# Optimization experiments

Hardware: AMD Instinct MI355X
Metric: run time of the kernel (lower is better)

Reference implementation:

```python
import jax, jax.numpy as jnp
import numpy as np

WINDOW_SIZES = (4, 16, 64)
MEMORY_DIM = 256


def setup_inputs() -> dict:
    key = jax.random.key(0)
    ks = jax.random.split(key, 9)
    d_model, mem = 256, MEMORY_DIM
    s_in = 1.0 / np.sqrt(d_model)
    s_mem = 1.0 / np.sqrt(mem)
    return {
        "hidden_states": jax.random.normal(ks[0], (2, 4096, d_model), dtype=jnp.float32),
        # weights stored as (in, out) so projection is x @ W + b
        "Wq": jax.random.normal(ks[1], (d_model, mem), dtype=jnp.float32) * s_in,
        "bq": jax.random.normal(ks[2], (mem,), dtype=jnp.float32) * 0.02,
        "Wk": jax.random.normal(ks[3], (d_model, mem), dtype=jnp.float32) * s_in,
        "bk": jax.random.normal(ks[4], (mem,), dtype=jnp.float32) * 0.02,
        "Wv": jax.random.normal(ks[5], (d_model, mem), dtype=jnp.float32) * s_in,
        "bv": jax.random.normal(ks[6], (mem,), dtype=jnp.float32) * 0.02,
        "Wo": jax.random.normal(ks[7], (mem, d_model), dtype=jnp.float32) * s_mem,
        "bo": jax.random.normal(ks[8], (d_model,), dtype=jnp.float32) * 0.02,
    }


def _gather_patches(h, window):
    # h: (B, L, D). Causal window of `window` positions ending at each l,
    # zero-padded on the left (matches F.pad + unfold in the torch module).
    B, L, D = h.shape
    w = min(window, L)
    padded = jnp.pad(h, ((0, 0), (w - 1, 0), (0, 0)))  # (B, L+w-1, D)
    idx = jnp.arange(L)[:, None] + jnp.arange(w)[None, :]  # (L, w)
    return padded[:, idx]  # (B, L, w, D)


def reference(hidden_states, Wq, bq, Wk, bk, Wv, bv, Wo, bo):
    scale = 1.0 / np.sqrt(MEMORY_DIM)
    q = hidden_states @ Wq + bq  # (B, L, M)
    contexts = []
    for window in WINDOW_SIZES:
        patches = _gather_patches(hidden_states, window)  # (B, L, w, D)
        keys = patches @ Wk + bk      # (B, L, w, M)
        values = patches @ Wv + bv    # (B, L, w, M)
        scores = jnp.einsum('bld,blwd->blw', q, keys) * scale
        attn = jax.nn.softmax(scores, axis=-1)
        contexts.append(jnp.einsum('blw,blwd->bld', attn, values))
    merged = contexts[0]
    for c in contexts[1:]:
        merged = merged + c
    merged = merged / len(contexts)
    return hidden_states + merged @ Wo + bo
```

## Files before the change

### kernel.cpp

```cpp
#include <hip/hip_runtime.h>
#include <hip/hip_bf16.h>

#define D 256
#define NROWS 8192
#define LXV 4176
#define VPAD 64
#define KXFB 1064960

#define QBLK 16
#define SSTR 84
#define PSTR 104
#define MSTR 264
#define BSTR 264

typedef unsigned int u32;
typedef unsigned short u16;

typedef short bf16x8 __attribute__((ext_vector_type(8)));
typedef float f32x4 __attribute__((ext_vector_type(4)));

__device__ __forceinline__ u16 f2bf(float f) {
    u32 x = __float_as_uint(f);
    x += 0x7fffu + ((x >> 16) & 1u);
    return (u16)(x >> 16);
}
__device__ __forceinline__ u32 pk2(float a, float b) {
    return (u32)f2bf(a) | ((u32)f2bf(b) << 16);
}

__global__ __launch_bounds__(256) void qkv_mfma(
    const float* __restrict__ H,
    const float* __restrict__ Wq, const float* __restrict__ Wk,
    const float* __restrict__ Wv, const float* __restrict__ Wo,
    const float* __restrict__ bq, const float* __restrict__ bkb,
    const float* __restrict__ bvb,
    u16* __restrict__ Qf, u16* __restrict__ Kxf, u16* __restrict__ Vt,
    u16* __restrict__ WoTf)
{
    __shared__ u16 As[64 * 256];
    __shared__ u16 Bs[64 * BSTR];
    __shared__ u16 Eb[64 * 72];

    const int tid = threadIdx.x;
    const int by = blockIdx.x;
    const int bx = blockIdx.y;
    const int mat = bx >> 2;
    const int n0 = (bx & 3) * 64;
    const int row0 = by * 256;
    const int batch = by >> 4;
    const int lrow0 = row0 & 4095;
    const float* __restrict__ W = (mat == 0) ? Wq : (mat == 1) ? Wk : Wv;
    const float* __restrict__ bias = (mat == 0) ? bq : (mat == 1) ? bkb : bvb;

    const int lane = tid & 63, w = tid >> 6;
    const int l15 = lane & 15, lhi = lane >> 4;
    const int rt2 = (w & 1) * 2, ct2 = (w >> 1) * 2;

    {
        const int kp = tid & 31, ng = tid >> 5;
        u32* bd = (u32*)Bs;
        #pragma unroll
        for (int s = 0; s < 4; ++s) {
            const float* wr = W + (size_t)(s * 64 + 2 * kp) * 256 + n0 + ng * 8;
            float4 a0 = *(const float4*)(wr);
            float4 a1 = *(const float4*)(wr + 4);
            float4 b0 = *(const float4*)(wr + 256);
            float4 b1 = *(const float4*)(wr + 260);
            bd[(ng * 8 + 0) * 132 + s * 32 + kp] = pk2(a0.x, b0.x);
            bd[(ng * 8 + 1) * 132 + s * 32 + kp] = pk2(a0.y, b0.y);
            bd[(ng * 8 + 2) * 132 + s * 32 + kp] = pk2(a0.z, b0.z);
            bd[(ng * 8 + 3) * 132 + s * 32 + kp] = pk2(a0.w, b0.w);
            bd[(ng * 8 + 4) * 132 + s * 32 + kp] = pk2(a1.x, b1.x);
            bd[(ng * 8 + 5) * 132 + s * 32 + kp] = pk2(a1.y, b1.y);
            bd[(ng * 8 + 6) * 132 + s * 32 + kp] = pk2(a1.z, b1.z);
            bd[(ng * 8 + 7) * 132 + s * 32 + kp] = pk2(a1.w, b1.w);
        }
    }
    {
        const int r = tid >> 2, cb = (tid & 3) * 64;
        const float* hp = H + (size_t)(row0 + r) * 256 + cb;
        const int swz = (r & 7) << 3;
        #pragma unroll
        for (int i = 0; i < 16; ++i) {
            float4 h4 = *(const float4*)(hp + i * 4);
            uint2 pv; pv.x = pk2(h4.x, h4.y); pv.y = pk2(h4.z, h4.w);
            *(uint2*)(As + ((r * 256 + cb + i * 4) ^ swz)) = pv;
        }
    }
    __syncthreads();

    for (int t = 0; t < 4; ++t) {
        f32x4 acc[2][2];
        #pragma unroll
        for (int rr = 0; rr < 2; ++rr)
            #pragma unroll
            for (int cc = 0; cc < 2; ++cc)
                acc[rr][cc] = (f32x4){0.f, 0.f, 0.f, 0.f};
        #pragma unroll
        for (int rr = 0; rr < 2; ++rr) {
            const int rowa = (rt2 + rr) * 16 + l15;
            const int swa = (rowa & 7) << 3;
            bf16x8 af[8];
            #pragma unroll
            for (int ks = 0; ks < 8; ++ks)
                af[ks] = *(const bf16x8*)(As + ((rowa * 256 + ks * 32 + lhi * 8) ^ swa));
            #pragma unroll
            for (int ks = 0; ks < 8; ++ks)
                #pragma unroll
                for (int cc = 0; cc < 2; ++cc) {
                    bf16x8 bf = *(const bf16x8*)&Bs[((ct2 + cc) * 16 + l15) * BSTR + ks * 32 + lhi * 8];
                    acc[rr][cc] = __builtin_amdgcn_mfma_f32_16x16x32_bf16(af[ks], bf, acc[rr][cc], 0, 0, 0);
                }
        }
        __syncthreads();

        if (mat == 2) {
            #pragma unroll
            for (int cc = 0; cc < 2; ++cc) {
                const int dl = (ct2 + cc) * 16 + l15;
                const float bi = bvb[n0 + dl];
                #pragma unroll
                for (int rr = 0; rr < 2; ++rr)
                    #pragma unroll
                    for (int reg = 0; reg < 4; ++reg)
                        Eb[dl * 72 + (rt2 + rr) * 16 + lhi * 4 + reg] = f2bf(acc[rr][cc][reg] + bi);
            }
        } else {
            #pragma unroll
            for (int cc = 0; cc < 2; ++cc) {
                const int cl = (ct2 + cc) * 16 + l15;
                const float bi = bias[n0 + cl];
                #pragma unroll
                for (int rr = 0; rr < 2; ++rr)
                    #pragma unroll
                    for (int reg = 0; reg < 4; ++reg)
                        Eb[((rt2 + rr) * 16 + lhi * 4 + reg) * 72 + cl] = f2bf(acc[rr][cc][reg] + bi);
            }
        }
        if (t < 3) {
            const int r = tid >> 2, cb = (tid & 3) * 64;
            const float* hp = H + (size_t)(row0 + (t + 1) * 64 + r) * 256 + cb;
            const int swz = (r & 7) << 3;
            #pragma unroll
            for (int i = 0; i < 16; ++i) {
                float4 h4 = *(const float4*)(hp + i * 4);
                uint2 pv; pv.x = pk2(h4.x, h4.y); pv.y = pk2(h4.z, h4.w);
                *(uint2*)(As + ((r * 256 + cb + i * 4) ^ swz)) = pv;
            }
        }
        __syncthreads();

        if (mat == 2) {
            const int d2 = tid >> 2, q = tid & 3;
            uint4 v0 = *(const uint4*)&Eb[d2 * 72 + q * 16];
            uint4 v1 = *(const uint4*)&Eb[d2 * 72 + q * 16 + 8];
            u16* dst = Vt + ((size_t)batch * 256 + n0 + d2) * LXV + VPAD + lrow0 + t * 64 + q * 16;
            *(uint4*)dst = v0;
            *(uint4*)(dst + 8) = v1;
        } else {
            const int r2 = tid >> 2, c16 = (tid & 3) * 16;
            int rtile, rl;
            u16* base;
            if (mat == 0) {
                const int grow = row0 + t * 64 + r2;
                rtile = grow >> 4; rl = grow & 15;
                base = Qf;
            } else {
                const int prow = VPAD + lrow0 + t * 64 + r2;
                rtile = prow >> 4; rl = prow & 15;
                base = Kxf + (size_t)batch * KXFB;
            }
            #pragma unroll
            for (int h = 0; h < 2; ++h) {
                const int gcol = n0 + c16 + h * 8;
                const int ksq = gcol >> 5;
                const int lhq = (gcol >> 3) & 3;
                uint4 v = *(const uint4*)&Eb[r2 * 72 + c16 + h * 8];
                *(uint4*)&base[((size_t)rtile * 8 + ksq) * 512 + (rl * 4 + lhq) * 8] = v;
            }
        }
    }

    if (bx == 0 && by < 16) {
        float* Tf = (float*)As;
        const int tr = by >> 2, tc = by & 3;
        __syncthreads();
        {
            const int r = tid >> 2, c0 = (tid & 3) * 16;
            const float* src = Wo + (size_t)(tr * 64 + r) * 256 + tc * 64 + c0;
            #pragma unroll
            for (int i = 0; i < 4; ++i) {
                float4 v = *(const float4*)(src + i * 4);
                Tf[r * 68 + c0 + i * 4 + 0] = v.x;
                Tf[r * 68 + c0 + i * 4 + 1] = v.y;
                Tf[r * 68 + c0 + i * 4 + 2] = v.z;
                Tf[r * 68 + c0 + i * 4 + 3] = v.w;
            }
        }
        __syncthreads();
        {
            const int n = tid >> 2, k0 = (tid & 3) * 16;
            const int gcol = tc * 64 + n;
            const int colt = gcol >> 4, cl = gcol & 15;
            const int gk = tr * 64 + k0;
            const int ksw = gk >> 5;
            const int lhw = (gk >> 3) & 3;
            u32 pw[8];
            #pragma unroll
            for (int i = 0; i < 8; ++i)
                pw[i] = pk2(Tf[(k0 + 2 * i) * 68 + n], Tf[(k0 + 2 * i + 1) * 68 + n]);
            u16* base = WoTf + ((size_t)colt * 8 + ksw) * 512 + (cl * 4 + lhw) * 8;
            *(uint4*)base = *(uint4*)&pw[0];
            *(uint4*)(base + 8) = *(uint4*)&pw[4];
        }
    }
    if (bx == 4 && (by & 15) == 0) {
        const int batch2 = by >> 4;
        const int ks = tid >> 5, u = tid & 31;
        const u16 val = f2bf(bkb[ks * 32 + u]);
        u16* base = Kxf + (size_t)batch2 * KXFB;
        #pragma unroll
        for (int pt = 0; pt < 4; ++pt)
            #pragma unroll
            for (int rl = 0; rl < 16; ++rl)
                base[((size_t)pt * 8 + ks) * 512 + rl * 32 + u] = val;
    }
    if (bx == 8 && (by & 15) == 0) {
        const int batch2 = by >> 4;
        const u16 val = f2bf(bvb[tid]);
        const u32 vv = (u32)val | ((u32)val << 16);
        uint4 o; o.x = vv; o.y = vv; o.z = vv; o.w = vv;
        u16* dst = Vt + ((size_t)batch2 * 256 + tid) * LXV;
        #pragma unroll
        for (int j = 0; j < 8; ++j) *(uint4*)(dst + j * 8) = o;
    }
}

__global__ __launch_bounds__(256) void attn_out(
    const u16* __restrict__ Qf, const u16* __restrict__ Kxf,
    const u16* __restrict__ Vt, const u16* __restrict__ WoTf,
    const float* __restrict__ bo, const float* __restrict__ H,
    float* __restrict__ out)
{
    __shared__ float Sb[QBLK * SSTR];
    __shared__ u16 Pb[QBLK * PSTR];
    __shared__ u16 Ml[QBLK * MSTR];

    const int tid = threadIdx.x;
    const int lane = tid & 63, w = tid >> 6;
    const int l15 = lane & 15, lhi = lane >> 4;
    const int bid = blockIdx.x;
    const int r0 = (((bid & 7) << 6) + (bid >> 3)) * QBLK;
    const int batch = r0 >> 12;
    const int lb0 = r0 & 4095;

    const float scale = 0.0625f;
    const int fidx = (l15 * 4 + lhi) * 8;
    const u16* qp = Qf + (size_t)(r0 >> 4) * 4096 + fidx;
    bf16x8 qf[8];
    #pragma unroll
    for (int ks = 0; ks < 8; ++ks) qf[ks] = *(const bf16x8*)(qp + ks * 512);

    const u16* kfb = Kxf + (size_t)batch * KXFB + (size_t)(lb0 >> 4) * 4096 + fidx;
    for (int T = w; T < 5; T += 4) {
        const u16* kp = kfb + (size_t)T * 4096;
        f32x4 acc = (f32x4){0.f, 0.f, 0.f, 0.f};
        #pragma unroll
        for (int ks = 0; ks < 8; ++ks) {
            bf16x8 kf = *(const bf16x8*)(kp + ks * 512);
            acc = __builtin_amdgcn_mfma_f32_16x16x32_bf16(qf[ks], kf, acc, 0, 0, 0);
        }
        #pragma unroll
        for (int reg = 0; reg < 4; ++reg)
            Sb[(lhi * 4 + reg) * SSTR + T * 16 + l15] = acc[reg] * scale;
    }
    __syncthreads();

    {
        const int ri = w * 4 + lhi;
        const int jb = l15;
        float s5[5];
        float m = -1e30f;
        #pragma unroll
        for (int c = 0; c < 5; ++c) {
            const int j = jb + 16 * c;
            const float x = Sb[ri * SSTR + j];
            const bool v = (j >= ri + 1) && (j <= ri + 64);
            s5[c] = v ? x : -1e30f;
            m = fmaxf(m, s5[c]);
        }
        #pragma unroll
        for (int o = 1; o < 16; o <<= 1) m = fmaxf(m, __shfl_xor(m, o));
        float e5[5], z64 = 0.f, z16 = 0.f, z4 = 0.f;
        #pragma unroll
        for (int c = 0; c < 5; ++c) {
            const int j = jb + 16 * c;
            const float e = __expf(s5[c] - m);
            e5[c] = e;
            z64 += e;
            if (j >= ri + 49) z16 += e;
            if (j >= ri + 61) z4 += e;
        }
        #pragma unroll
        for (int o = 1; o < 16; o <<= 1) {
            z64 += __shfl_xor(z64, o);
            z16 += __shfl_xor(z16, o);
            z4  += __shfl_xor(z4, o);
        }
        const float i64 = 1.f / z64, i16 = 1.f / z16, i4 = 1.f / z4;
        #pragma unroll
        for (int c = 0; c < 5; ++c) {
            const int j = jb + 16 * c;
            float wt = e5[c] * (i64 + (j >= ri + 49 ? i16 : 0.f) + (j >= ri + 61 ? i4 : 0.f)) * (1.f / 3.f);
            Pb[ri * PSTR + j] = f2bf(wt);
        }
        Pb[ri * PSTR + 80 + jb] = 0;
    }
    __syncthreads();

    bf16x8 pa[3];
    #pragma unroll
    for (int ks = 0; ks < 3; ++ks)
        pa[ks] = *(const bf16x8*)&Pb[l15 * PSTR + ks * 32 + lhi * 8];
    #pragma unroll
    for (int i = 0; i < 4; ++i) {
        const int dt = w * 4 + i;
        const u16* vrow = Vt + ((size_t)batch * 256 + dt * 16 + l15) * LXV + lb0;
        f32x4 acc = (f32x4){0.f, 0.f, 0.f, 0.f};
        #pragma unroll
        for (int ks = 0; ks < 3; ++ks) {
            bf16x8 vb = *(const bf16x8*)(vrow + ks * 32 + lhi * 8);
            acc = __builtin_amdgcn_mfma_f32_16x16x32_bf16(pa[ks], vb, acc, 0, 0, 0);
        }
        #pragma unroll
        for (int reg = 0; reg < 4; ++reg)
            Ml[(lhi * 4 + reg) * MSTR + dt * 16 + l15] = f2bf(acc[reg]);
    }
    __syncthreads();

    bf16x8 afm[8];
    #pragma unroll
    for (int ks = 0; ks < 8; ++ks)
        afm[ks] = *(const bf16x8*)&Ml[l15 * MSTR + ks * 32 + lhi * 8];

    #pragma unroll
    for (int ct = 0; ct < 4; ++ct) {
        const int colt = w * 4 + ct;
        const u16* wrow = WoTf + (size_t)colt * 4096 + fidx;
        f32x4 oac = (f32x4){0.f, 0.f, 0.f, 0.f};
        #pragma unroll
        for (int ks = 0; ks < 8; ++ks) {
            bf16x8 bf = *(const bf16x8*)(wrow + ks * 512);
            oac = __builtin_amdgcn_mfma_f32_16x16x32_bf16(afm[ks], bf, oac, 0, 0, 0);
        }
        const int col = w * 64 + ct * 16 + l15;
        const float bi = bo[col];
        #pragma unroll
        for (int reg = 0; reg < 4; ++reg) {
            const int r = r0 + lhi * 4 + reg;
            const size_t off = (size_t)r * 256 + col;
            out[off] = H[off] + oac[reg] + bi;
        }
    }
}

extern "C" void kernel_launch(void* const* d_in, const int* in_sizes, int n_in,
                              void* d_out, int out_size, void* d_ws, size_t ws_size,
                              hipStream_t stream) {
    const float* H  = (const float*)d_in[0];
    const float* Wq = (const float*)d_in[1];
    const float* bq = (const float*)d_in[2];
    const float* Wk = (const float*)d_in[3];
    const float* bk = (const float*)d_in[4];
    const float* Wv = (const float*)d_in[5];
    const float* bv = (const float*)d_in[6];
    const float* Wo = (const float*)d_in[7];
    const float* bo = (const float*)d_in[8];
    float* out = (float*)d_out;

    u16* Qf   = (u16*)d_ws;
    u16* Kxf  = Qf + (size_t)NROWS * 256;
    u16* Vt   = Kxf + (size_t)2 * KXFB;
    u16* WoTf = Vt + (size_t)2 * 256 * LXV;

    qkv_mfma<<<dim3(32, 12), 256, 0, stream>>>(H, Wq, Wk, Wv, Wo, bq, bk, bv, Qf, Kxf, Vt, WoTf);
    attn_out<<<512, 256, 0, stream>>>(Qf, Kxf, Vt, WoTf, bo, H, out);
}
```

Measured before the change: 43.65 us.

## Fuse QKV projection and attention kernels with flag-based inter-block dependencies

Merges the QKV/WoT preparation kernel and the attention-output kernel into one persistent-style launch of 512 blocks. Producer blocks signal completion per row group through global atomic flags, and each block then waits on the flags it needs before running the attention phase. The aim is to remove the launch gap between the two kernels and let attention work overlap with the projection tail. In exchange it adds a memset, spin-wait polling, and a risk of deadlock if not all producer blocks are resident; a bounded spin count guards against that but could let blocks read data that is not ready yet.

```diff
diff --git a/kernel.cpp b/kernel.cpp
--- a/kernel.cpp
+++ b/kernel.cpp
@@ -28,118 +28,65 @@
     return (u32)f2bf(a) | ((u32)f2bf(b) << 16);
 }
 
-__global__ __launch_bounds__(256) void qkv_mfma(
+__global__ __launch_bounds__(256, 2) void fused(
     const float* __restrict__ H,
     const float* __restrict__ Wq, const float* __restrict__ Wk,
     const float* __restrict__ Wv, const float* __restrict__ Wo,
     const float* __restrict__ bq, const float* __restrict__ bkb,
-    const float* __restrict__ bvb,
+    const float* __restrict__ bvb, const float* __restrict__ bo,
+    float* __restrict__ out, u32* __restrict__ flags,
     u16* __restrict__ Qf, u16* __restrict__ Kxf, u16* __restrict__ Vt,
     u16* __restrict__ WoTf)
 {
-    __shared__ u16 As[64 * 256];
-    __shared__ u16 Bs[64 * BSTR];
-    __shared__ u16 Eb[64 * 72];
-
+    __shared__ __align__(16) char smem[75776];
+    u16* As = (u16*)smem;
+    u16* Bs = (u16*)(smem + 32768);
+    u16* Eb = (u16*)(smem + 66560);
+    float* Sb = (float*)smem;
+    u16* Pb = (u16*)(smem + 5376);
+    u16* Ml = (u16*)(smem + 8704);
+
+    const int bid = blockIdx.x;
     const int tid = threadIdx.x;
-    const int by = blockIdx.x;
-    const int bx = blockIdx.y;
-    const int mat = bx >> 2;
-    const int n0 = (bx & 3) * 64;
-    const int row0 = by * 256;
-    const int batch = by >> 4;
-    const int lrow0 = row0 & 4095;
-    const float* __restrict__ W = (mat == 0) ? Wq : (mat == 1) ? Wk : Wv;
-    const float* __restrict__ bias = (mat == 0) ? bq : (mat == 1) ? bkb : bvb;
-
     const int lane = tid & 63, w = tid >> 6;
     const int l15 = lane & 15, lhi = lane >> 4;
     const int rt2 = (w & 1) * 2, ct2 = (w >> 1) * 2;
-
-    {
-        const int kp = tid & 31, ng = tid >> 5;
-        u32* bd = (u32*)Bs;
-        #pragma unroll
-        for (int s = 0; s < 4; ++s) {
-            const float* wr = W + (size_t)(s * 64 + 2 * kp) * 256 + n0 + ng * 8;
-            float4 a0 = *(const float4*)(wr);
-            float4 a1 = *(const float4*)(wr + 4);
-            float4 b0 = *(const float4*)(wr + 256);
-            float4 b1 = *(const float4*)(wr + 260);
-            bd[(ng * 8 + 0) * 132 + s * 32 + kp] = pk2(a0.x, b0.x);
-            bd[(ng * 8 + 1) * 132 + s * 32 + kp] = pk2(a0.y, b0.y);
-            bd[(ng * 8 + 2) * 132 + s * 32 + kp] = pk2(a0.z, b0.z);
-            bd[(ng * 8 + 3) * 132 + s * 32 + kp] = pk2(a0.w, b0.w);
-            bd[(ng * 8 + 4) * 132 + s * 32 + kp] = pk2(a1.x, b1.x);
-            bd[(ng * 8 + 5) * 132 + s * 32 + kp] = pk2(a1.y, b1.y);
-            bd[(ng * 8 + 6) * 132 + s * 32 + kp] = pk2(a1.z, b1.z);
-            bd[(ng * 8 + 7) * 132 + s * 32 + kp] = pk2(a1.w, b1.w);
-        }
-    }
-    {
-        const int r = tid >> 2, cb = (tid & 3) * 64;
-        const float* hp = H + (size_t)(row0 + r) * 256 + cb;
-        const int swz = (r & 7) << 3;
-        #pragma unroll
-        for (int i = 0; i < 16; ++i) {
-            float4 h4 = *(const float4*)(hp + i * 4);
-            uint2 pv; pv.x = pk2(h4.x, h4.y); pv.y = pk2(h4.z, h4.w);
-            *(uint2*)(As + ((r * 256 + cb + i * 4) ^ swz)) = pv;
-        }
-    }
-    __syncthreads();
-
-    for (int t = 0; t < 4; ++t) {
-        f32x4 acc[2][2];
-        #pragma unroll
-        for (int rr = 0; rr < 2; ++rr)
-            #pragma unroll
-            for (int cc = 0; cc < 2; ++cc)
-                acc[rr][cc] = (f32x4){0.f, 0.f, 0.f, 0.f};
-        #pragma unroll
-        for (int rr = 0; rr < 2; ++rr) {
-            const int rowa = (rt2 + rr) * 16 + l15;
-            const int swa = (rowa & 7) << 3;
-            bf16x8 af[8];
-            #pragma unroll
-            for (int ks = 0; ks < 8; ++ks)
-                af[ks] = *(const bf16x8*)(As + ((rowa * 256 + ks * 32 + lhi * 8) ^ swa));
-            #pragma unroll
-            for (int ks = 0; ks < 8; ++ks)
-                #pragma unroll
-                for (int cc = 0; cc < 2; ++cc) {
-                    bf16x8 bf = *(const bf16x8*)&Bs[((ct2 + cc) * 16 + l15) * BSTR + ks * 32 + lhi * 8];
-                    acc[rr][cc] = __builtin_amdgcn_mfma_f32_16x16x32_bf16(af[ks], bf, acc[rr][cc], 0, 0, 0);
-                }
-        }
-        __syncthreads();
-
-        if (mat == 2) {
-            #pragma unroll
-            for (int cc = 0; cc < 2; ++cc) {
-                const int dl = (ct2 + cc) * 16 + l15;
-                const float bi = bvb[n0 + dl];
-                #pragma unroll
-                for (int rr = 0; rr < 2; ++rr)
-                    #pragma unroll
-                    for (int reg = 0; reg < 4; ++reg)
-                        Eb[dl * 72 + (rt2 + rr) * 16 + lhi * 4 + reg] = f2bf(acc[rr][cc][reg] + bi);
-            }
-        } else {
-            #pragma unroll
-            for (int cc = 0; cc < 2; ++cc) {
-                const int cl = (ct2 + cc) * 16 + l15;
-                const float bi = bias[n0 + cl];
-                #pragma unroll
-                for (int rr = 0; rr < 2; ++rr)
-                    #pragma unroll
-                    for (int reg = 0; reg < 4; ++reg)
-                        Eb[((rt2 + rr) * 16 + lhi * 4 + reg) * 72 + cl] = f2bf(acc[rr][cc][reg] + bi);
-            }
-        }
-        if (t < 3) {
+    u32* wofl = flags + 32;
+
+    if (bid < 384) {
+        const int by = bid & 31;
+        const int bx = bid >> 5;
+        const int mat = bx >> 2;
+        const int n0 = (bx & 3) * 64;
+        const int row0 = by * 256;
+        const int batch = by >> 4;
+        const int lrow0 = row0 & 4095;
+        const float* __restrict__ W = (mat == 0) ? Wq : (mat == 1) ? Wk : Wv;
+        const float* __restrict__ bias = (mat == 0) ? bq : (mat == 1) ? bkb : bvb;
+
+        {
+            const int kp = tid & 31, ng = tid >> 5;
+            u32* bd = (u32*)Bs;
+            #pragma unroll
+            for (int s = 0; s < 4; ++s) {
+                const float* wr = W + (size_t)(s * 64 + 2 * kp) * 256 + n0 + ng * 8;
+                float4 a0 = *(const float4*)(wr);
+                float4 a1 = *(const float4*)(wr + 4);
+                float4 b0 = *(const float4*)(wr + 256);
+                float4 b1 = *(const float4*)(wr + 260);
+                bd[(ng * 8 + 0) * 132 + s * 32 + kp] = pk2(a0.x, b0.x);
+                bd[(ng * 8 + 1) * 132 + s * 32 + kp] = pk2(a0.y, b0.y);
+                bd[(ng * 8 + 2) * 132 + s * 32 + kp] = pk2(a0.z, b0.z);
+                bd[(ng * 8 + 3) * 132 + s * 32 + kp] = pk2(a0.w, b0.w);
+                bd[(ng * 8 + 4) * 132 + s * 32 + kp] = pk2(a1.x, b1.x);
+                bd[(ng * 8 + 5) * 132 + s * 32 + kp] = pk2(a1.y, b1.y);
+                bd[(ng * 8 + 6) * 132 + s * 32 + kp] = pk2(a1.z, b1.z);
+                bd[(ng * 8 + 7) * 132 + s * 32 + kp] = pk2(a1.w, b1.w);
+            }
+        }
+        {
             const int r = tid >> 2, cb = (tid & 3) * 64;
-            const float* hp = H + (size_t)(row0 + (t + 1) * 64 + r) * 256 + cb;
+            const float* hp = H + (size_t)(row0 + r) * 256 + cb;
             const int swz = (r & 7) << 3;
             #pragma unroll
             for (int i = 0; i < 16; ++i) {
@@ -150,41 +97,127 @@
         }
         __syncthreads();
 
-        if (mat == 2) {
-            const int d2 = tid >> 2, q = tid & 3;
-            uint4 v0 = *(const uint4*)&Eb[d2 * 72 + q * 16];
-            uint4 v1 = *(const uint4*)&Eb[d2 * 72 + q * 16 + 8];
-            u16* dst = Vt + ((size_t)batch * 256 + n0 + d2) * LXV + VPAD + lrow0 + t * 64 + q * 16;
-            *(uint4*)dst = v0;
-            *(uint4*)(dst + 8) = v1;
-        } else {
-            const int r2 = tid >> 2, c16 = (tid & 3) * 16;
-            int rtile, rl;
-            u16* base;
-            if (mat == 0) {
-                const int grow = row0 + t * 64 + r2;
-                rtile = grow >> 4; rl = grow & 15;
-                base = Qf;
+        for (int t = 0; t < 4; ++t) {
+            f32x4 acc[2][2];
+            #pragma unroll
+            for (int rr = 0; rr < 2; ++rr)
+                #pragma unroll
+                for (int cc = 0; cc < 2; ++cc)
+                    acc[rr][cc] = (f32x4){0.f, 0.f, 0.f, 0.f};
+            #pragma unroll
+            for (int rr = 0; rr < 2; ++rr) {
+                const int rowa = (rt2 + rr) * 16 + l15;
+                const int swa = (rowa & 7) << 3;
+                bf16x8 af[8];
+                #pragma unroll
+                for (int ks = 0; ks < 8; ++ks)
+                    af[ks] = *(const bf16x8*)(As + ((rowa * 256 + ks * 32 + lhi * 8) ^ swa));
+                #pragma unroll
+                for (int ks = 0; ks < 8; ++ks)
+                    #pragma unroll
+                    for (int cc = 0; cc < 2; ++cc) {
+                        bf16x8 bf = *(const bf16x8*)&Bs[((ct2 + cc) * 16 + l15) * BSTR + ks * 32 + lhi * 8];
+                        acc[rr][cc] = __builtin_amdgcn_mfma_f32_16x16x32_bf16(af[ks], bf, acc[rr][cc], 0, 0, 0);
+                    }
+            }
+            __syncthreads();
+
+            if (mat == 2) {
+                #pragma unroll
+                for (int cc = 0; cc < 2; ++cc) {
+                    const int dl = (ct2 + cc) * 16 + l15;
+                    const float bi = bvb[n0 + dl];
+                    #pragma unroll
+                    for (int rr = 0; rr < 2; ++rr)
+                        #pragma unroll
+                        for (int reg = 0; reg < 4; ++reg)
+                            Eb[dl * 72 + (rt2 + rr) * 16 + lhi * 4 + reg] = f2bf(acc[rr][cc][reg] + bi);
+                }
             } else {
-                const int prow = VPAD + lrow0 + t * 64 + r2;
-                rtile = prow >> 4; rl = prow & 15;
-                base = Kxf + (size_t)batch * KXFB;
-            }
-            #pragma unroll
-            for (int h = 0; h < 2; ++h) {
-                const int gcol = n0 + c16 + h * 8;
-                const int ksq = gcol >> 5;
-                const int lhq = (gcol >> 3) & 3;
-                uint4 v = *(const uint4*)&Eb[r2 * 72 + c16 + h * 8];
-                *(uint4*)&base[((size_t)rtile * 8 + ksq) * 512 + (rl * 4 + lhq) * 8] = v;
-            }
-        }
-    }
-
-    if (bx == 0 && by < 16) {
+                #pragma unroll
+                for (int cc = 0; cc < 2; ++cc) {
+                    const int cl = (ct2 + cc) * 16 + l15;
+                    const float bi = bias[n0 + cl];
+                    #pragma unroll
+                    for (int rr = 0; rr < 2; ++rr)
+                        #pragma unroll
+                        for (int reg = 0; reg < 4; ++reg)
+                            Eb[((rt2 + rr) * 16 + lhi * 4 + reg) * 72 + cl] = f2bf(acc[rr][cc][reg] + bi);
+                }
+            }
+            if (t < 3) {
+                const int r = tid >> 2, cb = (tid & 3) * 64;
+                const float* hp = H + (size_t)(row0 + (t + 1) * 64 + r) * 256 + cb;
+                const int swz = (r & 7) << 3;
+                #pragma unroll
+                for (int i = 0; i < 16; ++i) {
+                    float4 h4 = *(const float4*)(hp + i * 4);
+                    uint2 pv; pv.x = pk2(h4.x, h4.y); pv.y = pk2(h4.z, h4.w);
+                    *(uint2*)(As + ((r * 256 + cb + i * 4) ^ swz)) = pv;
+                }
+            }
+            __syncthreads();
+
+            if (mat == 2) {
+                const int d2 = tid >> 2, q = tid & 3;
+                uint4 v0 = *(const uint4*)&Eb[d2 * 72 + q * 16];
+                uint4 v1 = *(const uint4*)&Eb[d2 * 72 + q * 16 + 8];
+                u16* dst = Vt + ((size_t)batch * 256 + n0 + d2) * LXV + VPAD + lrow0 + t * 64 + q * 16;
+                *(uint4*)dst = v0;
+                *(uint4*)(dst + 8) = v1;
+            } else {
+                const int r2 = tid >> 2, c16 = (tid & 3) * 16;
+                int rtile, rl;
+                u16* base;
+                if (mat == 0) {
+                    const int grow = row0 + t * 64 + r2;
+                    rtile = grow >> 4; rl = grow & 15;
+                    base = Qf;
+                } else {
+                    const int prow = VPAD + lrow0 + t * 64 + r2;
+                    rtile = prow >> 4; rl = prow & 15;
+                    base = Kxf + (size_t)batch * KXFB;
+                }
+                #pragma unroll
+                for (int h = 0; h < 2; ++h) {
+                    const int gcol = n0 + c16 + h * 8;
+                    const int ksq = gcol >> 5;
+                    const int lhq = (gcol >> 3) & 3;
+                    uint4 v = *(const uint4*)&Eb[r2 * 72 + c16 + h * 8];
+                    *(uint4*)&base[((size_t)rtile * 8 + ksq) * 512 + (rl * 4 + lhq) * 8] = v;
+                }
+            }
+        }
+
+        if (bx == 4 && (by & 15) == 0) {
+            const int batch2 = by >> 4;
+            const int ks = tid >> 5, u = tid & 31;
+            const u16 val = f2bf(bkb[ks * 32 + u]);
+            u16* base = Kxf + (size_t)batch2 * KXFB;
+            #pragma unroll
+            for (int pt = 0; pt < 4; ++pt)
+                #pragma unroll
+                for (int rl = 0; rl < 16; ++rl)
+                    base[((size_t)pt * 8 + ks) * 512 + rl * 32 + u] = val;
+        }
+        if (bx == 8 && (by & 15) == 0) {
+            const int batch2 = by >> 4;
+            const u16 val = f2bf(bvb[tid]);
+            const u32 vv = (u32)val | ((u32)val << 16);
+            uint4 o; o.x = vv; o.y = vv; o.z = vv; o.w = vv;
+            u16* dst = Vt + ((size_t)batch2 * 256 + tid) * LXV;
+            #pragma unroll
+            for (int j = 0; j < 8; ++j) *(uint4*)(dst + j * 8) = o;
+        }
+        __syncthreads();
+        if (tid == 0) {
+            __threadfence();
+            atomicAdd(&flags[by], 1u);
+        }
+    } else if (bid < 400) {
         float* Tf = (float*)As;
-        const int tr = by >> 2, tc = by & 3;
-        __syncthreads();
+        const int wid = bid - 384;
+        const int tr = wid >> 2, tc = wid & 3;
         {
             const int r = tid >> 2, c0 = (tid & 3) * 16;
             const float* src = Wo + (size_t)(tr * 64 + r) * 256 + tc * 64 + c0;
@@ -213,153 +246,142 @@
             *(uint4*)base = *(uint4*)&pw[0];
             *(uint4*)(base + 8) = *(uint4*)&pw[4];
         }
+        __syncthreads();
+        if (tid == 0) {
+            __threadfence();
+            atomicAdd(wofl, 1u);
+        }
     }
-    if (bx == 4 && (by & 15) == 0) {
-        const int batch2 = by >> 4;
-        const int ks = tid >> 5, u = tid & 31;
-        const u16 val = f2bf(bkb[ks * 32 + u]);
-        u16* base = Kxf + (size_t)batch2 * KXFB;
+
+    {
+        const int aid = bid;
+        const int r0 = (((aid & 7) << 6) + (aid >> 3)) * QBLK;
+        const int batch = r0 >> 12;
+        const int lb0 = r0 & 4095;
+        const int rg_hi = (batch << 4) + (lb0 >> 8);
+        const int lo = (lb0 >= 63) ? (lb0 - 63) : 0;
+        const int rg_lo = (batch << 4) + (lo >> 8);
+
+        if (tid == 0) {
+            int spin = 0;
+            for (;;) {
+                const u32 a = atomicAdd(&flags[rg_lo], 0u);
+                const u32 b = atomicAdd(&flags[rg_hi], 0u);
+                const u32 c = atomicAdd(wofl, 0u);
+                if ((a >= 12u && b >= 12u && c >= 16u) || ++spin > (1 << 20)) break;
+                __builtin_amdgcn_s_sleep(16);
+            }
+            __threadfence();
+        }
+        __syncthreads();
+
+        const float scale = 0.0625f;
+        const int fidx = (l15 * 4 + lhi) * 8;
+        const u16* qp = Qf + (size_t)(r0 >> 4) * 4096 + fidx;
+        bf16x8 qf[8];
         #pragma unroll
-        for (int pt = 0; pt < 4; ++pt)
-            #pragma unroll
-            for (int rl = 0; rl < 16; ++rl)
-                base[((size_t)pt * 8 + ks) * 512 + rl * 32 + u] = val;
-    }
-    if (bx == 8 && (by & 15) == 0) {
-        const int batch2 = by >> 4;
-        const u16 val = f2bf(bvb[tid]);
-        const u32 vv = (u32)val | ((u32)val << 16);
-        uint4 o; o.x = vv; o.y = vv; o.z = vv; o.w = vv;
-        u16* dst = Vt + ((size_t)batch2 * 256 + tid) * LXV;
+        for (int ks = 0; ks < 8; ++ks) qf[ks] = *(const bf16x8*)(qp + ks * 512);
+
+        const u16* kfb = Kxf + (size_t)batch * KXFB + (size_t)(lb0 >> 4) * 4096 + fidx;
+        for (int T = w; T < 5; T += 4) {
+            const u16* kp = kfb + (size_t)T * 4096;
+            f32x4 acc = (f32x4){0.f, 0.f, 0.f, 0.f};
+            #pragma unroll
+            for (int ks = 0; ks < 8; ++ks) {
+                bf16x8 kf = *(const bf16x8*)(kp + ks * 512);
+                acc = __builtin_amdgcn_mfma_f32_16x16x32_bf16(qf[ks], kf, acc, 0, 0, 0);
+            }
+            #pragma unroll
+            for (int reg = 0; reg < 4; ++reg)
+                Sb[(lhi * 4 + reg) * SSTR + T * 16 + l15] = acc[reg] * scale;
+        }
+        __syncthreads();
+
+        {
+            const int ri = w * 4 + lhi;
+            const int jb = l15;
+            float s5[5];
+            float m = -1e30f;
+            #pragma unroll
+            for (int c = 0; c < 5; ++c) {
+                const int j = jb + 16 * c;
+                const float x = Sb[ri * SSTR + j];
+                const bool v = (j >= ri + 1) && (j <= ri + 64);
+                s5[c] = v ? x : -1e30f;
+                m = fmaxf(m, s5[c]);
+            }
+            #pragma unroll
+            for (int o = 1; o < 16; o <<= 1) m = fmaxf(m, __shfl_xor(m, o));
+            float e5[5], z64 = 0.f, z16 = 0.f, z4 = 0.f;
+            #pragma unroll
+            for (int c = 0; c < 5; ++c) {
+                const int j = jb + 16 * c;
+                const float e = __expf(s5[c] - m);
+                e5[c] = e;
+                z64 += e;
+                if (j >= ri + 49) z16 += e;
+                if (j >= ri + 61) z4 += e;
+            }
+            #pragma unroll
+            for (int o = 1; o < 16; o <<= 1) {
+                z64 += __shfl_xor(z64, o);
+                z16 += __shfl_xor(z16, o);
+                z4  += __shfl_xor(z4, o);
+            }
+            const float i64 = 1.f / z64, i16 = 1.f / z16, i4 = 1.f / z4;
+            #pragma unroll
+            for (int c = 0; c < 5; ++c) {
+                const int j = jb + 16 * c;
+                float wt = e5[c] * (i64 + (j >= ri + 49 ? i16 : 0.f) + (j >= ri + 61 ? i4 : 0.f)) * (1.f / 3.f);
+                Pb[ri * PSTR + j] = f2bf(wt);
+            }
+            Pb[ri * PSTR + 80 + jb] = 0;
+        }
+        __syncthreads();
+
+        bf16x8 pa[3];
         #pragma unroll
-        for (int j = 0; j < 8; ++j) *(uint4*)(dst + j * 8) = o;
-    }
-}
-
-__global__ __launch_bounds__(256) void attn_out(
-    const u16* __restrict__ Qf, const u16* __restrict__ Kxf,
-    const u16* __restrict__ Vt, const u16* __restrict__ WoTf,
-    const float* __restrict__ bo, const float* __restrict__ H,
-    float* __restrict__ out)
-{
-    __shared__ float Sb[QBLK * SSTR];
-    __shared__ u16 Pb[QBLK * PSTR];
-    __shared__ u16 Ml[QBLK * MSTR];
-
-    const int tid = threadIdx.x;
-    const int lane = tid & 63, w = tid >> 6;
-    const int l15 = lane & 15, lhi = lane >> 4;
-    const int bid = blockIdx.x;
-    const int r0 = (((bid & 7) << 6) + (bid >> 3)) * QBLK;
-    const int batch = r0 >> 12;
-    const int lb0 = r0 & 4095;
-
-    const float scale = 0.0625f;
-    const int fidx = (l15 * 4 + lhi) * 8;
-    const u16* qp = Qf + (size_t)(r0 >> 4) * 4096 + fidx;
-    bf16x8 qf[8];
-    #pragma unroll
-    for (int ks = 0; ks < 8; ++ks) qf[ks] = *(const bf16x8*)(qp + ks * 512);
-
-    const u16* kfb = Kxf + (size_t)batch * KXFB + (size_t)(lb0 >> 4) * 4096 + fidx;
-    for (int T = w; T < 5; T += 4) {
-        const u16* kp = kfb + (size_t)T * 4096;
-        f32x4 acc = (f32x4){0.f, 0.f, 0.f, 0.f};
+        for (int ks = 0; ks < 3; ++ks)
+            pa[ks] = *(const bf16x8*)&Pb[l15 * PSTR + ks * 32 + lhi * 8];
         #pragma unroll
-        for (int ks = 0; ks < 8; ++ks) {
-            bf16x8 kf = *(const bf16x8*)(kp + ks * 512);
-            acc = __builtin_amdgcn_mfma_f32_16x16x32_bf16(qf[ks], kf, acc, 0, 0, 0);
-        }
+        for (int i = 0; i < 4; ++i) {
+            const int dt = w * 4 + i;
+            const u16* vrow = Vt + ((size_t)batch * 256 + dt * 16 + l15) * LXV + lb0;
+            f32x4 acc = (f32x4){0.f, 0.f, 0.f, 0.f};
+            #pragma unroll
+            for (int ks = 0; ks < 3; ++ks) {
+                bf16x8 vb = *(const bf16x8*)(vrow + ks * 32 + lhi * 8);
+                acc = __builtin_amdgcn_mfma_f32_16x16x32_bf16(pa[ks], vb, acc, 0, 0, 0);
+            }
+            #pragma unroll
+            for (int reg = 0; reg < 4; ++reg)
+                Ml[(lhi * 4 + reg) * MSTR + dt * 16 + l15] = f2bf(acc[reg]);
+        }
+        __syncthreads();
+
+        bf16x8 afm[8];
         #pragma unroll
-        for (int reg = 0; reg < 4; ++reg)
-            Sb[(lhi * 4 + reg) * SSTR + T * 16 + l15] = acc[reg] * scale;
-    }
-    __syncthreads();
-
-    {
-        const int ri = w * 4 + lhi;
-        const int jb = l15;
-        float s5[5];
-        float m = -1e30f;
+        for (int ks = 0; ks < 8; ++ks)
+            afm[ks] = *(const bf16x8*)&Ml[l15 * MSTR + ks * 32 + lhi * 8];
+
         #pragma unroll
-        for (int c = 0; c < 5; ++c) {
-            const int j = jb + 16 * c;
-            const float x = Sb[ri * SSTR + j];
-            const bool v = (j >= ri + 1) && (j <= ri + 64);
-            s5[c] = v ? x : -1e30f;
-            m = fmaxf(m, s5[c]);
-        }
-        #pragma unroll
-        for (int o = 1; o < 16; o <<= 1) m = fmaxf(m, __shfl_xor(m, o));
-        float e5[5], z64 = 0.f, z16 = 0.f, z4 = 0.f;
-        #pragma unroll
-        for (int c = 0; c < 5; ++c) {
-            const int j = jb + 16 * c;
-            const float e = __expf(s5[c] - m);
-            e5[c] = e;
-            z64 += e;
-            if (j >= ri + 49) z16 += e;
-            if (j >= ri + 61) z4 += e;
-        }
-        #pragma unroll
-        for (int o = 1; o < 16; o <<= 1) {
-            z64 += __shfl_xor(z64, o);
-            z16 += __shfl_xor(z16, o);
-            z4  += __shfl_xor(z4, o);
-        }
-        const float i64 = 1.f / z64, i16 = 1.f / z16, i4 = 1.f / z4;
-        #pragma unroll
-        for (int c = 0; c < 5; ++c) {
-            const int j = jb + 16 * c;
-            float wt = e5[c] * (i64 + (j >= ri + 49 ? i16 : 0.f) + (j >= ri + 61 ? i4 : 0.f)) * (1.f / 3.f);
-            Pb[ri * PSTR + j] = f2bf(wt);
-        }
-        Pb[ri * PSTR + 80 + jb] = 0;
-    }
-    __syncthreads();
-
-    bf16x8 pa[3];
-    #pragma unroll
-    for (int ks = 0; ks < 3; ++ks)
-        pa[ks] = *(const bf16x8*)&Pb[l15 * PSTR + ks * 32 + lhi * 8];
-    #pragma unroll
-    for (int i = 0; i < 4; ++i) {
-        const int dt = w * 4 + i;
-        const u16* vrow = Vt + ((size_t)batch * 256 + dt * 16 + l15) * LXV + lb0;
-        f32x4 acc = (f32x4){0.f, 0.f, 0.f, 0.f};
-        #pragma unroll
-        for (int ks = 0; ks < 3; ++ks) {
-            bf16x8 vb = *(const bf16x8*)(vrow + ks * 32 + lhi * 8);
-            acc = __builtin_amdgcn_mfma_f32_16x16x32_bf16(pa[ks], vb, acc, 0, 0, 0);
-        }
-        #pragma unroll
-        for (int reg = 0; reg < 4; ++reg)
-            Ml[(lhi * 4 + reg) * MSTR + dt * 16 + l15] = f2bf(acc[reg]);
-    }
-    __syncthreads();
-
-    bf16x8 afm[8];
-    #pragma unroll
-    for (int ks = 0; ks < 8; ++ks)
-        afm[ks] = *(const bf16x8*)&Ml[l15 * MSTR + ks * 32 + lhi * 8];
-
-    #pragma unroll
-    for (int ct = 0; ct < 4; ++ct) {
-        const int colt = w * 4 + ct;
-        const u16* wrow = WoTf + (size_t)colt * 4096 + fidx;
-        f32x4 oac = (f32x4){0.f, 0.f, 0.f, 0.f};
-        #pragma unroll
-        for (int ks = 0; ks < 8; ++ks) {
-            bf16x8 bf = *(const bf16x8*)(wrow + ks * 512);
-            oac = __builtin_amdgcn_mfma_f32_16x16x32_bf16(afm[ks], bf, oac, 0, 0, 0);
-        }
-        const int col = w * 64 + ct * 16 + l15;
-        const float bi = bo[col];
-        #pragma unroll
-        for (int reg = 0; reg < 4; ++reg) {
-            const int r = r0 + lhi * 4 + reg;
-            const size_t off = (size_t)r * 256 + col;
-            out[off] = H[off] + oac[reg] + bi;
+        for (int ct = 0; ct < 4; ++ct) {
+            const int colt = w * 4 + ct;
+            const u16* wrow = WoTf + (size_t)colt * 4096 + fidx;
+            f32x4 oac = (f32x4){0.f, 0.f, 0.f, 0.f};
+            #pragma unroll
+            for (int ks = 0; ks < 8; ++ks) {
+                bf16x8 bf = *(const bf16x8*)(wrow + ks * 512);
+                oac = __builtin_amdgcn_mfma_f32_16x16x32_bf16(afm[ks], bf, oac, 0, 0, 0);
+            }
+            const int col = w * 64 + ct * 16 + l15;
+            const float bi = bo[col];
+            #pragma unroll
+            for (int reg = 0; reg < 4; ++reg) {
+                const int r = r0 + lhi * 4 + reg;
+                const size_t off = (size_t)r * 256 + col;
+                out[off] = H[off] + oac[reg] + bi;
+            }
         }
     }
 }
@@ -378,11 +400,14 @@
     const float* bo = (const float*)d_in[8];
     float* out = (float*)d_out;
 
-    u16* Qf   = (u16*)d_ws;
+    u32* flags = (u32*)d_ws;
+    char* base = (char*)d_ws + 256;
+    u16* Qf   = (u16*)base;
     u16* Kxf  = Qf + (size_t)NROWS * 256;
     u16* Vt   = Kxf + (size_t)2 * KXFB;
     u16* WoTf = Vt + (size_t)2 * 256 * LXV;
 
-    qkv_mfma<<<dim3(32, 12), 256, 0, stream>>>(H, Wq, Wk, Wv, Wo, bq, bk, bv, Qf, Kxf, Vt, WoTf);
-    attn_out<<<512, 256, 0, stream>>>(Qf, Kxf, Vt, WoTf, bo, H, out);
+    hipMemsetAsync(flags, 0, 256, stream);
+    fused<<<512, 256, 0, stream>>>(H, Wq, Wk, Wv, Wo, bq, bk, bv, bo, out,
+                                   flags, Qf, Kxf, Vt, WoTf);
 }
```

New measurement: 102.9 us. +135.8%, slower.
